# Performance work log

Hardware: AMD Instinct MI355X
Metric: run time of the kernel (lower is better)

## Reference

```python
import jax, jax.numpy as jnp
import numpy as np

D = 16        # flow dimensionality (args.d)
M = 128       # hidden nodes per layer
L = 2         # num_hidden_layers
B = 256       # batch
NF = 2        # num_flows
NORM_C = 1.0  # get_normalizing_const for initialization='sqrt-(m)'
STD_H = 1.0 / np.sqrt(M)  # give_std('sqrt-(m)', M)
STD_A = 0.1   # std for last layer


def _lower_mask(out, inp, d):
    # block lower-triangular (incl. diagonal) mask over d x d blocks
    return jnp.kron(jnp.tril(jnp.ones((d, d), jnp.float32)), jnp.ones((out // d, inp // d), jnp.float32))


def _diag_blocks(W, d):
    # extract the d diagonal blocks of W -> (d, out_blk, in_blk)
    ob, ib = W.shape[0] // d, W.shape[1] // d
    idx = jnp.arange(d)
    return W.reshape(d, ob, d, ib)[idx, :, idx, :]


def _init_W(key, out, inp, d, std):
    # 'clamp-zero' init: positive diagonal blocks, gaussian strictly-lower blocks, zero above
    W = std * jax.random.normal(key, (out, inp), dtype=jnp.float32)
    lm = _lower_mask(out, inp, d)
    dm = jnp.kron(jnp.eye(d, dtype=jnp.float32), jnp.ones((out // d, inp // d), jnp.float32))
    W = W * lm
    return jnp.where(dm > 0, jnp.clip(jnp.abs(W), 1e-10, None), W)


def _flow(inp, Ws, bs, d, norm_c):
    b = inp.shape[0]
    out, grad = inp, None
    nlay = len(bs)
    log_c = jnp.log(jnp.asarray(norm_c, inp.dtype))
    for i in range(nlay):
        W = Ws[i]
        wm = W * _lower_mask(W.shape[0], W.shape[1], d)
        lg = jnp.log(_diag_blocks(W, d))            # (d, ob, ib)
        if grad is None:
            grad = jnp.broadcast_to(lg[None], (b,) + lg.shape)  # (B, d, ob, 1)
        else:
            # log-space matvec over previous width: (B,d,ob,1)
            grad = jax.nn.logsumexp(lg[None, :, :, :, None] + grad[:, :, None, :, :], axis=3)
        out = out @ wm.T + bs[i]                    # (B, ob*d)
        # log |tanh'(out)| = 2*(log2 - out - softplus(-2 out))
        lga = 2.0 * (jnp.log(2.0) - out - jax.nn.softplus(-2.0 * out))
        out = norm_c * jnp.tanh(out)
        ob = W.shape[0] // d
        grad = grad + lga.reshape(b, d, ob, 1) + log_c
    # final (linear) layer
    W = Ws[nlay]
    wm = W * _lower_mask(W.shape[0], W.shape[1], d)
    lg = jnp.log(_diag_blocks(W, d))                # (d, 1, ib)
    grad = jax.nn.logsumexp(lg[None, :, :, :, None] + grad[:, :, None, :, :], axis=3)  # (B,d,1,1)
    out = out @ wm.T                                # (B, d)
    return out, grad.reshape(b, d).sum(-1)          # log-det Jacobian per sample


def setup_inputs() -> dict:
    key = jax.random.key(0)
    ks = jax.random.split(key, 11)
    inp = jax.random.normal(ks[0], (B, D), dtype=jnp.float32)
    params = {}
    for f in range(NF):
        o = 1 + 5 * f
        params[f'f{f}_W0'] = _init_W(ks[o + 0], M * D, D, D, STD_H)
        params[f'f{f}_W1'] = _init_W(ks[o + 1], M * D, M * D, D, STD_H)
        params[f'f{f}_W2'] = _init_W(ks[o + 2], D, M * D, D, STD_A)
        params[f'f{f}_b0'] = STD_H * jax.random.normal(ks[o + 3], (M * D,), dtype=jnp.float32)
        params[f'f{f}_b1'] = STD_H * jax.random.normal(ks[o + 4], (M * D,), dtype=jnp.float32)
    return {'inp': inp, **params}


def reference(inp, f0_W0, f0_W1, f0_W2, f0_b0, f0_b1, f1_W0, f1_W1, f1_W2, f1_b0, f1_b1):
    out, ld0 = _flow(inp, [f0_W0, f0_W1, f0_W2], [f0_b0, f0_b1], D, NORM_C)
    out, ld1 = _flow(out, [f1_W0, f1_W1, f1_W2], [f1_b0, f1_b1], D, NORM_C)
    return out, ld0 + ld1
```

## Files before the change

kernel.cpp:

```cpp
#include <hip/hip_runtime.h>
#include <stdint.h>

#define BATCH 256
#define DBLK  16
#define OB    128
#define NN    2048

using bf16x8  = __attribute__((ext_vector_type(8))) __bf16;
using f32x4   = __attribute__((ext_vector_type(4))) float;
using ushort8 = __attribute__((ext_vector_type(8))) unsigned short;

__device__ __forceinline__ unsigned short f2bf(float f) {
    union { float f; uint32_t u; } v; v.f = f;
    uint32_t u = v.u;
    uint32_t r = (u + 0x7fffu + ((u >> 16) & 1u)) >> 16;
    return (unsigned short)r;
}

__device__ __forceinline__ float bf2f(unsigned short h) {
    union { uint32_t u; float f; } v; v.u = ((uint32_t)h) << 16;
    return v.f;
}

__device__ __forceinline__ void act_tanh_lga(float x, float& th, float& lga) {
    float ax = fabsf(x);
    float e  = __expf(-2.f * ax);
    float p  = 1.f + e;
    float t  = 1.f - __fdividef(2.f * e, p);
    th  = (x < 0.f) ? -t : t;
    lga = 2.f * (0.69314718055994531f - ax - __logf(p));
}

__device__ __forceinline__ ushort8 pack_bf8(float4 a, float4 b) {
    ushort8 u;
    u[0] = f2bf(a.x); u[1] = f2bf(a.y); u[2] = f2bf(a.z); u[3] = f2bf(a.w);
    u[4] = f2bf(b.x); u[5] = f2bf(b.y); u[6] = f2bf(b.z); u[7] = f2bf(b.w);
    return u;
}

__device__ __forceinline__ void conv8pairs(int cid, int tid,
                                           const float* __restrict__ Wsrc,
                                           unsigned short* __restrict__ Wdst) {
    float4 va[5][2];
    unsigned short* dp[5];
    bool act[5];
    #pragma unroll
    for (int i = 0; i < 5; ++i) {
        const int c = tid + i * 512;
        act[i] = (c < 2176);
        if (act[i]) {
            const int pi  = c / 272;
            const int rem = c - pi * 272;
            const int p   = cid * 8 + pi;
            const int kend0 = ((p >> 7) + 1) * OB;
            const int off = rem * 8;
            const int row = (off < kend0) ? p : (NN - 1 - p);
            const int k   = (off < kend0) ? off : (off - kend0);
            const float* sp = Wsrc + (size_t)row * NN + k;
            dp[i] = Wdst + (size_t)row * NN + k;
            va[i][0] = *(const float4*)(sp);
            va[i][1] = *(const float4*)(sp + 4);
        }
    }
    #pragma unroll
    for (int i = 0; i < 5; ++i)
        if (act[i]) *(ushort8*)dp[i] = pack_bf8(va[i][0], va[i][1]);
}

__device__ __forceinline__ void l0_block512(const float* __restrict__ xs,
                                            const float* __restrict__ W0,
                                            const float* __restrict__ b0,
                                            unsigned short* __restrict__ h0,
                                            unsigned short* __restrict__ e0,
                                            float* __restrict__ mmax,
                                            int b, int t) {
    const int dd = t >> 5;
    const int j0 = dd * OB + (t & 31) * 4;
    float g[4];
    unsigned short hv[4];
    float lm = -1e30f;
    #pragma unroll
    for (int q = 0; q < 4; ++q) {
        const int j = j0 + q;
        const float* wrow = W0 + (size_t)j * DBLK;
        float s = b0[j];
        #pragma unroll
        for (int c = 0; c < DBLK; c += 4) {
            float4 wv = *(const float4*)(wrow + c);
            s += wv.x * xs[c] + wv.y * xs[c + 1] + wv.z * xs[c + 2] + wv.w * xs[c + 3];
        }
        float th, lga;
        act_tanh_lga(s, th, lga);
        hv[q] = f2bf(th);
        g[q]  = __logf(wrow[dd]) + lga;
        lm = fmaxf(lm, g[q]);
    }
    #pragma unroll
    for (int off = 1; off < 32; off <<= 1) lm = fmaxf(lm, __shfl_xor(lm, off));
    ushort4 hh, ee;
    #pragma unroll
    for (int q = 0; q < 4; ++q) {
        ((unsigned short*)&hh)[q] = hv[q];
        ((unsigned short*)&ee)[q] = f2bf(__expf(g[q] - lm));
    }
    *(ushort4*)(h0 + (size_t)b * NN + j0) = hh;
    *(ushort4*)(e0 + (size_t)b * NN + j0) = ee;
    if ((t & 31) == 0) mmax[b * DBLK + dd] = lm;
}

__global__ void __launch_bounds__(512)
k_prep(const float* __restrict__ W1a,
       unsigned short* __restrict__ W1bf,
       const float* __restrict__ inp,
       const float* __restrict__ W00,
       const float* __restrict__ b00,
       unsigned short* __restrict__ h0,
       unsigned short* __restrict__ e0,
       float* __restrict__ mmax) {
    const int gb = blockIdx.x;
    const int t  = threadIdx.x;
    if (gb < 128) {
        conv8pairs(gb, t, W1a, W1bf);
    } else {
        const int b = gb - 128;
        l0_block512(inp + (size_t)b * DBLK, W00, b00, h0, e0, mmax, b, t);
    }
}

template<bool CONV>
__global__ void __launch_bounds__(512, 2)
k_l1(const unsigned short* __restrict__ h0,
     const unsigned short* __restrict__ W1b,
     const float* __restrict__ b1v,
     const unsigned short* __restrict__ e0,
     const float* __restrict__ mmax,
     unsigned short* __restrict__ h1,
     float* __restrict__ g1,
     const float* __restrict__ W1next,
     unsigned short* __restrict__ W1bfn) {
    const int tid = threadIdx.x;

    int dd;
    if (CONV) {
        if (blockIdx.x < 4) {
            const int cid = (int)blockIdx.x * 32 + (int)blockIdx.y * 4 + (int)blockIdx.z;
            conv8pairs(cid, tid, W1next, W1bfn);
            return;
        }
        dd = 19 - (int)blockIdx.x;
    } else {
        dd = 15 - (int)blockIdx.x;
    }
    const int btp   = blockIdx.y;
    const int ct    = blockIdx.z;
    const int w     = tid >> 6;
    const int lane  = tid & 63;
    const int brow0 = btp * 32;
    const int arow0 = brow0 + (lane & 15);
    const int arow1 = arow0 + 16;
    const int koff  = (lane >> 4) * 8;
    const int ncol  = lane & 15;
    const int col0  = dd * OB + ct * 32;

    f32x4 acc[2][2], acc2[2][2];
    #pragma unroll
    for (int hh = 0; hh < 2; ++hh)
        #pragma unroll
        for (int nt = 0; nt < 2; ++nt) {
            acc[hh][nt]  = (f32x4){0.f, 0.f, 0.f, 0.f};
            acc2[hh][nt] = (f32x4){0.f, 0.f, 0.f, 0.f};
        }

    const unsigned short* Ab0 = h0 + (size_t)arow0 * NN + koff;
    const unsigned short* Ab1 = h0 + (size_t)arow1 * NN + koff;
    const unsigned short* Bb[2];
    #pragma unroll
    for (int nt = 0; nt < 2; ++nt)
        Bb[nt] = W1b + (size_t)(col0 + nt * 16 + ncol) * NN + koff;

    bf16x8 ga0 = {}, ga1 = {}, gb0 = {}, gb1 = {};
    if (w < 4) {
        const int k2 = dd * OB + w * 32;
        ga0 = *(const bf16x8*)(e0 + (size_t)arow0 * NN + koff + k2);
        ga1 = *(const bf16x8*)(e0 + (size_t)arow1 * NN + koff + k2);
        gb0 = *(const bf16x8*)(Bb[0] + k2);
        gb1 = *(const bf16x8*)(Bb[1] + k2);
    }

    const int nch = (dd + 1) * 4;
    #pragma unroll 2
    for (int c = w; c < nch; c += 8) {
        const int k = c * 32;
        bf16x8 a0  = *(const bf16x8*)(Ab0 + k);
        bf16x8 a1  = *(const bf16x8*)(Ab1 + k);
        bf16x8 b0v = *(const bf16x8*)(Bb[0] + k);
        bf16x8 b1w = *(const bf16x8*)(Bb[1] + k);
        acc[0][0] = __builtin_amdgcn_mfma_f32_16x16x32_bf16(a0, b0v, acc[0][0], 0, 0, 0);
        acc[0][1] = __builtin_amdgcn_mfma_f32_16x16x32_bf16(a0, b1w, acc[0][1], 0, 0, 0);
        acc[1][0] = __builtin_amdgcn_mfma_f32_16x16x32_bf16(a1, b0v, acc[1][0], 0, 0, 0);
        acc[1][1] = __builtin_amdgcn_mfma_f32_16x16x32_bf16(a1, b1w, acc[1][1], 0, 0, 0);
    }

    if (w < 4) {
        acc2[0][0] = __builtin_amdgcn_mfma_f32_16x16x32_bf16(ga0, gb0, acc2[0][0], 0, 0, 0);
        acc2[0][1] = __builtin_amdgcn_mfma_f32_16x16x32_bf16(ga0, gb1, acc2[0][1], 0, 0, 0);
        acc2[1][0] = __builtin_amdgcn_mfma_f32_16x16x32_bf16(ga1, gb0, acc2[1][0], 0, 0, 0);
        acc2[1][1] = __builtin_amdgcn_mfma_f32_16x16x32_bf16(ga1, gb1, acc2[1][1], 0, 0, 0);
    }

    __shared__ float ls1[8][2][2][64][4];
    __shared__ float ls2[4][2][2][64][4];
    #pragma unroll
    for (int hh = 0; hh < 2; ++hh)
        #pragma unroll
        for (int nt = 0; nt < 2; ++nt)
            *(f32x4*)&ls1[w][hh][nt][lane][0] = acc[hh][nt];
    if (w < 4) {
        #pragma unroll
        for (int hh = 0; hh < 2; ++hh)
            #pragma unroll
            for (int nt = 0; nt < 2; ++nt)
                *(f32x4*)&ls2[w][hh][nt][lane][0] = acc2[hh][nt];
    }
    __syncthreads();

    #pragma unroll
    for (int half = 0; half < 2; ++half) {
        const int o   = tid;
        const int rr2 = o >> 5;
        const int cc  = o & 31;
        const int nt  = cc >> 4;
        const int r   = rr2 & 3;
        const int ls  = (rr2 >> 2) * 16 + (cc & 15);
        float S = 0.f, S2 = 0.f;
        #pragma unroll
        for (int ww = 0; ww < 8; ++ww) S += ls1[ww][half][nt][ls][r];
        #pragma unroll
        for (int ww = 0; ww < 4; ++ww) S2 += ls2[ww][half][nt][ls][r];
        const int j    = col0 + cc;
        const int brow = brow0 + half * 16 + rr2;
        const float pre = S + b1v[j];
        float th, lga;
        act_tanh_lga(pre, th, lga);
        h1[(size_t)brow * NN + j] = f2bf(th);
        g1[(size_t)brow * NN + j] = __logf(S2) + mmax[brow * DBLK + dd] + lga;
    }
}

__device__ __forceinline__ float final_compute(const unsigned short* __restrict__ h1,
                                               const float* __restrict__ g1,
                                               const float* __restrict__ W2,
                                               int b, int t,
                                               float* sh, float* gf, float* sx) {
    const int wave = t >> 6;
    const int lane = t & 63;
    {
        const int k = t * 4;
        ushort4 hv = *(const ushort4*)(h1 + (size_t)b * NN + k);
        float4 f0;
        f0.x = bf2f(hv.x); f0.y = bf2f(hv.y); f0.z = bf2f(hv.z); f0.w = bf2f(hv.w);
        *(float4*)(sh + k) = f0;
    }
    __syncthreads();

    #pragma unroll
    for (int q = 0; q < 2; ++q) {
        const int dd = wave + q * 8;
        const float* w2r = W2 + (size_t)dd * NN;
        const int kend = (dd + 1) * OB;
        float s = 0.f;
        for (int k = lane * 4; k < kend; k += 64 * 4) {
            float4 hv = *(const float4*)(sh + k);
            float4 wv = *(const float4*)(w2r + k);
            s += hv.x * wv.x + hv.y * wv.y + hv.z * wv.z + hv.w * wv.w;
        }
        #pragma unroll
        for (int off = 32; off > 0; off >>= 1) s += __shfl_xor(s, off);
        float v0 = g1[(size_t)b * NN + dd * OB + lane];
        float v1 = g1[(size_t)b * NN + dd * OB + 64 + lane];
        float m = fmaxf(v0, v1);
        #pragma unroll
        for (int off = 32; off > 0; off >>= 1) m = fmaxf(m, __shfl_xor(m, off));
        float e = __expf(v0 - m) * w2r[dd * OB + lane]
                + __expf(v1 - m) * w2r[dd * OB + 64 + lane];
        #pragma unroll
        for (int off = 32; off > 0; off >>= 1) e += __shfl_xor(e, off);
        if (lane == 0) {
            sx[dd] = s;
            gf[dd] = __logf(e) + m;
        }
    }
    __syncthreads();
    float ld = 0.f;
    #pragma unroll
    for (int dd = 0; dd < DBLK; ++dd) ld += gf[dd];
    return ld;
}

__global__ void __launch_bounds__(512)
k_fin0(const unsigned short* __restrict__ h1,
       const float* __restrict__ g1,
       const float* __restrict__ W2,
       const float* __restrict__ W0n,
       const float* __restrict__ b0n,
       unsigned short* __restrict__ h0,
       unsigned short* __restrict__ e0,
       float* __restrict__ mmax,
       float* __restrict__ ld0) {
    __shared__ float sh[NN];
    __shared__ float gf[DBLK];
    __shared__ float sx[DBLK];
    const int b = blockIdx.x;
    const int t = threadIdx.x;
    float ld = final_compute(h1, g1, W2, b, t, sh, gf, sx);
    if (t == 0) ld0[b] = ld;
    l0_block512(sx, W0n, b0n, h0, e0, mmax, b, t);
}

__global__ void __launch_bounds__(512)
k_fin1(const unsigned short* __restrict__ h1,
       const float* __restrict__ g1,
       const float* __restrict__ W2,
       const float* __restrict__ ld0,
       float* __restrict__ out_final,
       float* __restrict__ ld_final) {
    __shared__ float sh[NN];
    __shared__ float gf[DBLK];
    __shared__ float sx[DBLK];
    const int b = blockIdx.x;
    const int t = threadIdx.x;
    float ld = final_compute(h1, g1, W2, b, t, sh, gf, sx);
    if (t < DBLK) out_final[b * DBLK + t] = sx[t];
    if (t == 0) ld_final[b] = ld + ld0[b];
}

extern "C" void kernel_launch(void* const* d_in, const int* in_sizes, int n_in,
                              void* d_out, int out_size, void* d_ws, size_t ws_size,
                              hipStream_t stream) {
    const float* inp   = (const float*)d_in[0];
    const float* W0[2] = {(const float*)d_in[1], (const float*)d_in[6]};
    const float* W1[2] = {(const float*)d_in[2], (const float*)d_in[7]};
    const float* W2[2] = {(const float*)d_in[3], (const float*)d_in[8]};
    const float* b0[2] = {(const float*)d_in[4], (const float*)d_in[9]};
    const float* b1[2] = {(const float*)d_in[5], (const float*)d_in[10]};

    char* w = (char*)d_ws;
    size_t off = 0;
    unsigned short* W1bf = (unsigned short*)(w + off); off += (size_t)2 * NN * NN * 2;
    unsigned short* h0b  = (unsigned short*)(w + off); off += (size_t)BATCH * NN * 2;
    unsigned short* e0b  = (unsigned short*)(w + off); off += (size_t)BATCH * NN * 2;
    float* mmax = (float*)(w + off); off += (size_t)BATCH * DBLK * 4;
    unsigned short* h1 = (unsigned short*)(w + off); off += (size_t)BATCH * NN * 2;
    float* g1   = (float*)(w + off); off += (size_t)BATCH * NN * 4;
    float* ld0  = (float*)(w + off); off += (size_t)BATCH * 4;

    float* out_final = (float*)d_out;
    float* ld_final  = (float*)d_out + BATCH * DBLK;

    k_prep<<<dim3(384), dim3(512), 0, stream>>>(
        W1[0], W1bf, inp, W0[0], b0[0], h0b, e0b, mmax);

    k_l1<true><<<dim3(20, 8, 4), dim3(512), 0, stream>>>(
        h0b, W1bf, b1[0], e0b, mmax, h1, g1,
        W1[1], W1bf + (size_t)NN * NN);

    k_fin0<<<dim3(BATCH), dim3(512), 0, stream>>>(
        h1, g1, W2[0], W0[1], b0[1], h0b, e0b, mmax, ld0);

    k_l1<false><<<dim3(16, 8, 4), dim3(512), 0, stream>>>(
        h0b, W1bf + (size_t)NN * NN, b1[1], e0b, mmax, h1, g1,
        nullptr, nullptr);

    k_fin1<<<dim3(BATCH), dim3(512), 0, stream>>>(
        h1, g1, W2[1], ld0, out_final, ld_final);
}
```

Before: 76.75 us.

## Drop separate W1 bf16 conversion pass; convert fp32 weights inline in GEMM

Removes the precomputation that converted the lower-triangular part of each 2048x2048 W1 matrix to bf16 in a workspace, which was spread across the prep and first GEMM kernels. The GEMM kernel now reads the fp32 weights directly and converts them to bf16 in registers just before each MFMA. This saves the write and re-read of the bf16 copy and simplifies the launch schedule. In exchange the GEMM reads twice the weight bytes per tile, and each batch-tile block reloads them, so it can become more bandwidth bound.

```diff
diff --git a/kernel.cpp b/kernel.cpp
--- a/kernel.cpp
+++ b/kernel.cpp
@@ -20,6 +20,13 @@
 __device__ __forceinline__ float bf2f(unsigned short h) {
     union { uint32_t u; float f; } v; v.u = ((uint32_t)h) << 16;
     return v.f;
+}
+
+__device__ __forceinline__ bf16x8 cvt_bf8(float4 a, float4 b) {
+    bf16x8 r;
+    r[0] = (__bf16)a.x; r[1] = (__bf16)a.y; r[2] = (__bf16)a.z; r[3] = (__bf16)a.w;
+    r[4] = (__bf16)b.x; r[5] = (__bf16)b.y; r[6] = (__bf16)b.z; r[7] = (__bf16)b.w;
+    return r;
 }
 
 __device__ __forceinline__ void act_tanh_lga(float x, float& th, float& lga) {
@@ -29,42 +36,6 @@
     float t  = 1.f - __fdividef(2.f * e, p);
     th  = (x < 0.f) ? -t : t;
     lga = 2.f * (0.69314718055994531f - ax - __logf(p));
-}
-
-__device__ __forceinline__ ushort8 pack_bf8(float4 a, float4 b) {
-    ushort8 u;
-    u[0] = f2bf(a.x); u[1] = f2bf(a.y); u[2] = f2bf(a.z); u[3] = f2bf(a.w);
-    u[4] = f2bf(b.x); u[5] = f2bf(b.y); u[6] = f2bf(b.z); u[7] = f2bf(b.w);
-    return u;
-}
-
-__device__ __forceinline__ void conv8pairs(int cid, int tid,
-                                           const float* __restrict__ Wsrc,
-                                           unsigned short* __restrict__ Wdst) {
-    float4 va[5][2];
-    unsigned short* dp[5];
-    bool act[5];
-    #pragma unroll
-    for (int i = 0; i < 5; ++i) {
-        const int c = tid + i * 512;
-        act[i] = (c < 2176);
-        if (act[i]) {
-            const int pi  = c / 272;
-            const int rem = c - pi * 272;
-            const int p   = cid * 8 + pi;
-            const int kend0 = ((p >> 7) + 1) * OB;
-            const int off = rem * 8;
-            const int row = (off < kend0) ? p : (NN - 1 - p);
-            const int k   = (off < kend0) ? off : (off - kend0);
-            const float* sp = Wsrc + (size_t)row * NN + k;
-            dp[i] = Wdst + (size_t)row * NN + k;
-            va[i][0] = *(const float4*)(sp);
-            va[i][1] = *(const float4*)(sp + 4);
-        }
-    }
-    #pragma unroll
-    for (int i = 0; i < 5; ++i)
-        if (act[i]) *(ushort8*)dp[i] = pack_bf8(va[i][0], va[i][1]);
 }
 
 __device__ __forceinline__ void l0_block512(const float* __restrict__ xs,
@@ -109,48 +80,26 @@
 }
 
 __global__ void __launch_bounds__(512)
-k_prep(const float* __restrict__ W1a,
-       unsigned short* __restrict__ W1bf,
-       const float* __restrict__ inp,
-       const float* __restrict__ W00,
-       const float* __restrict__ b00,
-       unsigned short* __restrict__ h0,
-       unsigned short* __restrict__ e0,
-       float* __restrict__ mmax) {
-    const int gb = blockIdx.x;
-    const int t  = threadIdx.x;
-    if (gb < 128) {
-        conv8pairs(gb, t, W1a, W1bf);
-    } else {
-        const int b = gb - 128;
-        l0_block512(inp + (size_t)b * DBLK, W00, b00, h0, e0, mmax, b, t);
-    }
-}
-
-template<bool CONV>
+k_l0(const float* __restrict__ inp,
+     const float* __restrict__ W00,
+     const float* __restrict__ b00,
+     unsigned short* __restrict__ h0,
+     unsigned short* __restrict__ e0,
+     float* __restrict__ mmax) {
+    l0_block512(inp + (size_t)blockIdx.x * DBLK, W00, b00, h0, e0, mmax,
+                blockIdx.x, threadIdx.x);
+}
+
 __global__ void __launch_bounds__(512, 2)
 k_l1(const unsigned short* __restrict__ h0,
-     const unsigned short* __restrict__ W1b,
+     const float* __restrict__ W1f,
      const float* __restrict__ b1v,
      const unsigned short* __restrict__ e0,
      const float* __restrict__ mmax,
      unsigned short* __restrict__ h1,
-     float* __restrict__ g1,
-     const float* __restrict__ W1next,
-     unsigned short* __restrict__ W1bfn) {
+     float* __restrict__ g1) {
     const int tid = threadIdx.x;
-
-    int dd;
-    if (CONV) {
-        if (blockIdx.x < 4) {
-            const int cid = (int)blockIdx.x * 32 + (int)blockIdx.y * 4 + (int)blockIdx.z;
-            conv8pairs(cid, tid, W1next, W1bfn);
-            return;
-        }
-        dd = 19 - (int)blockIdx.x;
-    } else {
-        dd = 15 - (int)blockIdx.x;
-    }
+    const int dd  = 15 - (int)blockIdx.x;
     const int btp   = blockIdx.y;
     const int ct    = blockIdx.z;
     const int w     = tid >> 6;
@@ -173,18 +122,22 @@
 
     const unsigned short* Ab0 = h0 + (size_t)arow0 * NN + koff;
     const unsigned short* Ab1 = h0 + (size_t)arow1 * NN + koff;
-    const unsigned short* Bb[2];
+    const float* Bf[2];
     #pragma unroll
     for (int nt = 0; nt < 2; ++nt)
-        Bb[nt] = W1b + (size_t)(col0 + nt * 16 + ncol) * NN + koff;
+        Bf[nt] = W1f + (size_t)(col0 + nt * 16 + ncol) * NN + koff;
 
     bf16x8 ga0 = {}, ga1 = {}, gb0 = {}, gb1 = {};
     if (w < 4) {
         const int k2 = dd * OB + w * 32;
         ga0 = *(const bf16x8*)(e0 + (size_t)arow0 * NN + koff + k2);
         ga1 = *(const bf16x8*)(e0 + (size_t)arow1 * NN + koff + k2);
-        gb0 = *(const bf16x8*)(Bb[0] + k2);
-        gb1 = *(const bf16x8*)(Bb[1] + k2);
+        float4 g00 = *(const float4*)(Bf[0] + k2);
+        float4 g01 = *(const float4*)(Bf[0] + k2 + 4);
+        float4 g10 = *(const float4*)(Bf[1] + k2);
+        float4 g11 = *(const float4*)(Bf[1] + k2 + 4);
+        gb0 = cvt_bf8(g00, g01);
+        gb1 = cvt_bf8(g10, g11);
     }
 
     const int nch = (dd + 1) * 4;
@@ -193,8 +146,12 @@
         const int k = c * 32;
         bf16x8 a0  = *(const bf16x8*)(Ab0 + k);
         bf16x8 a1  = *(const bf16x8*)(Ab1 + k);
-        bf16x8 b0v = *(const bf16x8*)(Bb[0] + k);
-        bf16x8 b1w = *(const bf16x8*)(Bb[1] + k);
+        float4 c00 = *(const float4*)(Bf[0] + k);
+        float4 c01 = *(const float4*)(Bf[0] + k + 4);
+        float4 c10 = *(const float4*)(Bf[1] + k);
+        float4 c11 = *(const float4*)(Bf[1] + k + 4);
+        bf16x8 b0v = cvt_bf8(c00, c01);
+        bf16x8 b1w = cvt_bf8(c10, c11);
         acc[0][0] = __builtin_amdgcn_mfma_f32_16x16x32_bf16(a0, b0v, acc[0][0], 0, 0, 0);
         acc[0][1] = __builtin_amdgcn_mfma_f32_16x16x32_bf16(a0, b1w, acc[0][1], 0, 0, 0);
         acc[1][0] = __builtin_amdgcn_mfma_f32_16x16x32_bf16(a1, b0v, acc[1][0], 0, 0, 0);
@@ -346,7 +303,6 @@
 
     char* w = (char*)d_ws;
     size_t off = 0;
-    unsigned short* W1bf = (unsigned short*)(w + off); off += (size_t)2 * NN * NN * 2;
     unsigned short* h0b  = (unsigned short*)(w + off); off += (size_t)BATCH * NN * 2;
     unsigned short* e0b  = (unsigned short*)(w + off); off += (size_t)BATCH * NN * 2;
     float* mmax = (float*)(w + off); off += (size_t)BATCH * DBLK * 4;
@@ -357,19 +313,17 @@
     float* out_final = (float*)d_out;
     float* ld_final  = (float*)d_out + BATCH * DBLK;
 
-    k_prep<<<dim3(384), dim3(512), 0, stream>>>(
-        W1[0], W1bf, inp, W0[0], b0[0], h0b, e0b, mmax);
-
-    k_l1<true><<<dim3(20, 8, 4), dim3(512), 0, stream>>>(
-        h0b, W1bf, b1[0], e0b, mmax, h1, g1,
-        W1[1], W1bf + (size_t)NN * NN);
+    k_l0<<<dim3(BATCH), dim3(512), 0, stream>>>(
+        inp, W0[0], b0[0], h0b, e0b, mmax);
+
+    k_l1<<<dim3(16, 8, 4), dim3(512), 0, stream>>>(
+        h0b, W1[0], b1[0], e0b, mmax, h1, g1);
 
     k_fin0<<<dim3(BATCH), dim3(512), 0, stream>>>(
         h1, g1, W2[0], W0[1], b0[1], h0b, e0b, mmax, ld0);
 
-    k_l1<false><<<dim3(16, 8, 4), dim3(512), 0, stream>>>(
-        h0b, W1bf + (size_t)NN * NN, b1[1], e0b, mmax, h1, g1,
-        nullptr, nullptr);
+    k_l1<<<dim3(16, 8, 4), dim3(512), 0, stream>>>(
+        h0b, W1[1], b1[1], e0b, mmax, h1, g1);
 
     k_fin1<<<dim3(BATCH), dim3(512), 0, stream>>>(
         h1, g1, W2[1], ld0, out_final, ld_final);
```

Measured after the change: 83.71 us. 9.1% more time.
